# Performance work log

Measured on AMD Instinct MI355X. Metric: run time of the kernel, lower is better.

## Reference

```python
import jax, jax.numpy as jnp
import numpy as np

HEADS = 16
DIM_HEAD = 64
SCALE = DIM_HEAD ** -0.5
MASK_NEG = 1000000.0


def setup_inputs() -> dict:
    key = jax.random.key(0)
    ks = jax.random.split(key, 6)
    B, N, M, D = 2, 2048, 2048, 1024
    inner = HEADS * DIM_HEAD  # 1024
    x = jax.random.normal(ks[0], (B, N, D), dtype=jnp.float32)
    context = jax.random.normal(ks[1], (B, M, D), dtype=jnp.float32)
    mask = jax.random.randint(ks[2], (B, N), 0, 2, dtype=jnp.int32)
    Wq = jax.random.normal(ks[3], (D, inner), dtype=jnp.float32) * (D ** -0.5)
    Wkv = jax.random.normal(ks[4], (D, 2 * inner), dtype=jnp.float32) * (D ** -0.5)
    Wout = jax.random.normal(ks[5], (inner, D), dtype=jnp.float32) * (inner ** -0.5)
    bout = jnp.zeros((D,), dtype=jnp.float32)
    return {"x": x, "context": context, "mask": mask,
            "Wq": Wq, "Wkv": Wkv, "Wout": Wout, "bout": bout}


def _split_heads(t):
    # [b, n, (h d)] -> [b, h, n, d]
    b, n, _ = t.shape
    return t.reshape(b, n, HEADS, DIM_HEAD).transpose(0, 2, 1, 3)


def reference(x, context, mask, Wq, Wkv, Wout, bout):
    kv = context @ Wkv                      # [b, m, 2*inner]
    k, v = jnp.split(kv, 2, axis=-1)
    q = x @ Wq                              # [b, n, inner]
    q, k, v = _split_heads(q), _split_heads(k), _split_heads(v)
    dots = jnp.einsum('bhnd,bhmd->bhnm', q, k) * SCALE
    # mask is [b, n]: additive penalty per query row (faithful to source)
    dots = dots - (1.0 - mask.astype(jnp.float32))[:, None, :, None] * MASK_NEG
    attn = jax.nn.softmax(dots, axis=-1)
    out = jnp.einsum('bhnm,bhmd->bhnd', attn, v)  # [b, h, n, d]
    b, h, n, d = out.shape
    out = out.transpose(0, 2, 1, 3).reshape(b, n, h * d)
    return out @ Wout + bout
```

## Files before the change

### kernel.cpp

```cpp
#include <hip/hip_runtime.h>
#include <hip/hip_bf16.h>
#include <math.h>

#define BATCH   2
#define NQ      2048
#define NKV     2048
#define DMODEL  1024
#define HEADS   16
#define INNER   1024
#define KVCOLS  2048

typedef short bf16x8 __attribute__((ext_vector_type(8)));
typedef float f32x4  __attribute__((ext_vector_type(4)));

__device__ __forceinline__ short f2bf(float x) {
    __hip_bfloat16 h = __float2bfloat16(x);
    return *reinterpret_cast<short*>(&h);
}
__device__ __forceinline__ float bf2f(short h) {
    unsigned int u = ((unsigned int)(unsigned short)h) << 16;
    float f;
    __builtin_memcpy(&f, &u, 4);
    return f;
}
__device__ __forceinline__ void gl_lds16(const void* g, void* l) {
    __builtin_amdgcn_global_load_lds(
        (const __attribute__((address_space(1))) unsigned int*)g,
        (__attribute__((address_space(3))) unsigned int*)l, 16, 0, 0);
}
__device__ __forceinline__ int sw(int row, int chunk) {
    return row * 64 + ((chunk ^ (row & 7)) << 3);
}

__device__ __forceinline__ void split_chunk(const float* __restrict__ in,
                                            short* __restrict__ hi,
                                            short* __restrict__ lo, int id)
{
    const int i = (id * 256 + (int)threadIdx.x) * 4;
    float4 v = *(const float4*)(in + i);
    short4 h, l;
    h.x = f2bf(v.x); l.x = f2bf(v.x - bf2f(h.x));
    h.y = f2bf(v.y); l.y = f2bf(v.y - bf2f(h.y));
    h.z = f2bf(v.z); l.z = f2bf(v.z - bf2f(h.z));
    h.w = f2bf(v.w); l.w = f2bf(v.w - bf2f(h.w));
    *(short4*)(hi + i) = h;
    *(short4*)(lo + i) = l;
}

__device__ __forceinline__ void tile_transpose_split(
    const float* __restrict__ W, short* __restrict__ Wth, short* __restrict__ Wtl,
    int Kd, int Nd, int bx, int by, int split)
{
    __shared__ float t[32][33];
    const int lx = threadIdx.x & 31, ly = threadIdx.x >> 5;
    #pragma unroll
    for (int j = 0; j < 4; ++j)
        t[ly + j * 8][lx] = W[(size_t)(by * 32 + ly + j * 8) * Nd + bx * 32 + lx];
    __syncthreads();
    #pragma unroll
    for (int j = 0; j < 4; ++j) {
        const float v = t[lx][ly + j * 8];
        const short h = f2bf(v);
        const size_t idx = (size_t)(bx * 32 + ly + j * 8) * Kd + by * 32 + lx;
        Wth[idx] = h;
        if (split) Wtl[idx] = f2bf(v - bf2f(h));
    }
}

__global__ __launch_bounds__(256)
void prep_all(const float* __restrict__ x, const float* __restrict__ ctx,
              const float* __restrict__ Wq, const float* __restrict__ Wkv,
              const float* __restrict__ Wout,
              short* __restrict__ xh, short* __restrict__ xl,
              short* __restrict__ ch, short* __restrict__ cl,
              short* __restrict__ WqTh, short* __restrict__ WqTl,
              short* __restrict__ WkvTh, short* __restrict__ WkvTl,
              short* __restrict__ WoutT)
{
    const int id = blockIdx.x;
    if (id < 4096) {
        split_chunk(x, xh, xl, id);
    } else if (id < 8192) {
        split_chunk(ctx, ch, cl, id - 4096);
    } else {
        const int r = id - 8192;
        if (r < 1024)
            tile_transpose_split(Wq, WqTh, WqTl, 1024, 1024, r & 31, r >> 5, 1);
        else if (r < 3072)
            tile_transpose_split(Wkv, WkvTh, WkvTl, 1024, 2048, (r - 1024) & 63, (r - 1024) >> 6, 1);
        else
            tile_transpose_split(Wout, WoutT, nullptr, 1024, 1024, (r - 3072) & 31, (r - 3072) >> 5, 0);
    }
}

__global__ __launch_bounds__(256)
void qkv_gemm(const short* __restrict__ xh, const short* __restrict__ xl,
              const short* __restrict__ ch, const short* __restrict__ cl,
              const short* __restrict__ WqTh, const short* __restrict__ WqTl,
              const short* __restrict__ WkvTh, const short* __restrict__ WkvTl,
              short* __restrict__ qhp, short* __restrict__ qlp,
              short* __restrict__ khp, short* __restrict__ klp,
              short* __restrict__ vp)
{
    __shared__ short Ash[128 * 32];
    __shared__ short Asl[128 * 32];
    __shared__ short Bsh[128 * 32];
    __shared__ short Bsl[128 * 32];

    const int tid = threadIdx.x;
    const int z = blockIdx.z;
    const int m0 = blockIdx.y * 128, n0 = blockIdx.x * 128;
    const int w = tid >> 6, ln = tid & 63;
    const int wm = (w & 1) * 64, wn = (w >> 1) * 64;
    const int lr = ln & 15, lq = ln >> 4;
    const int terms = (z == 2) ? 1 : 3;

    const short* Ah  = (z == 0) ? xh : ch;
    const short* Al  = (z == 0) ? xl : cl;
    const short* Bth = (z == 0) ? WqTh : (z == 1 ? WkvTh : WkvTh + (size_t)1024 * 1024);
    const short* Btl = (z == 0) ? WqTl : WkvTl;

    f32x4 acc[4][4];
    #pragma unroll
    for (int mt = 0; mt < 4; ++mt)
        #pragma unroll
        for (int nt = 0; nt < 4; ++nt)
            #pragma unroll
            for (int r = 0; r < 4; ++r) acc[mt][nt][r] = 0.0f;

    for (int k0 = 0; k0 < 1024; k0 += 32) {
        __syncthreads();
        #pragma unroll
        for (int it = 0; it < 2; ++it) {
            const int f = it * 256 + tid;
            const int row = f >> 2, c = f & 3;
            const int cg = c ^ ((row >> 1) & 3);
            const size_t ao = (size_t)(m0 + row) * 1024 + k0 + cg * 8;
            const size_t bo = (size_t)(n0 + row) * 1024 + k0 + cg * 8;
            gl_lds16(Ah  + ao, Ash + f * 8);
            gl_lds16(Bth + bo, Bsh + f * 8);
            if (terms == 3) {
                gl_lds16(Al  + ao, Asl + f * 8);
                gl_lds16(Btl + bo, Bsl + f * 8);
            }
        }
        __syncthreads();

        bf16x8 ah[4], bh[4];
        #pragma unroll
        for (int t = 0; t < 4; ++t) {
            const int ar = wm + t * 16 + lr;
            const int br = wn + t * 16 + lr;
            ah[t] = *(const bf16x8*)(Ash + ar * 32 + ((lq ^ ((ar >> 1) & 3)) << 3));
            bh[t] = *(const bf16x8*)(Bsh + br * 32 + ((lq ^ ((br >> 1) & 3)) << 3));
        }
        #pragma unroll
        for (int mt = 0; mt < 4; ++mt)
            #pragma unroll
            for (int nt = 0; nt < 4; ++nt)
                acc[mt][nt] = __builtin_amdgcn_mfma_f32_16x16x32_bf16(
                    ah[mt], bh[nt], acc[mt][nt], 0, 0, 0);

        if (terms == 3) {
            bf16x8 al[4], bl[4];
            #pragma unroll
            for (int t = 0; t < 4; ++t) {
                const int ar = wm + t * 16 + lr;
                const int br = wn + t * 16 + lr;
                al[t] = *(const bf16x8*)(Asl + ar * 32 + ((lq ^ ((ar >> 1) & 3)) << 3));
                bl[t] = *(const bf16x8*)(Bsl + br * 32 + ((lq ^ ((br >> 1) & 3)) << 3));
            }
            #pragma unroll
            for (int mt = 0; mt < 4; ++mt)
                #pragma unroll
                for (int nt = 0; nt < 4; ++nt) {
                    acc[mt][nt] = __builtin_amdgcn_mfma_f32_16x16x32_bf16(
                        ah[mt], bl[nt], acc[mt][nt], 0, 0, 0);
                    acc[mt][nt] = __builtin_amdgcn_mfma_f32_16x16x32_bf16(
                        al[mt], bh[nt], acc[mt][nt], 0, 0, 0);
                }
        }
    }

    const float scale = (z == 0) ? 2.0f : 1.0f;
    short* Chi = (z == 0) ? qhp : (z == 1 ? khp : vp);
    short* Clo = (z == 0) ? qlp : klp;
    #pragma unroll
    for (int mt = 0; mt < 4; ++mt)
        #pragma unroll
        for (int nt = 0; nt < 4; ++nt)
            #pragma unroll
            for (int r = 0; r < 4; ++r) {
                const int row = m0 + wm + mt * 16 + lq * 4 + r;
                const int col = n0 + wn + nt * 16 + lr;
                const float v = acc[mt][nt][r] * scale;
                const short hh = f2bf(v);
                Chi[(size_t)row * 1024 + col] = hh;
                if (z != 2)
                    Clo[(size_t)row * 1024 + col] = f2bf(v - bf2f(hh));
            }
}

__global__ __launch_bounds__(256)
void gemm_out(const short* __restrict__ A, const short* __restrict__ Bt,
              float* __restrict__ C, const float* __restrict__ bias)
{
    __shared__ short As[128 * 64];
    __shared__ short Bs[64 * 64];
    const int tid = threadIdx.x;
    const int m0 = blockIdx.y * 128, n0 = blockIdx.x * 64;
    const int w = tid >> 6, ln = tid & 63;
    const int wm = (w & 1) * 64, wn = (w >> 1) * 32;
    const int lr = ln & 15, lq = ln >> 4;

    f32x4 acc[4][2];
    #pragma unroll
    for (int mt = 0; mt < 4; ++mt)
        #pragma unroll
        for (int nt = 0; nt < 2; ++nt)
            #pragma unroll
            for (int r = 0; r < 4; ++r) acc[mt][nt][r] = 0.0f;

    for (int k0 = 0; k0 < 1024; k0 += 64) {
        __syncthreads();
        #pragma unroll
        for (int it = 0; it < 4; ++it) {
            const int f = it * 256 + tid;
            const int row = f >> 3, c8 = f & 7;
            const int cg = c8 ^ (row & 7);
            gl_lds16(A + (size_t)(m0 + row) * 1024 + k0 + cg * 8, As + f * 8);
        }
        #pragma unroll
        for (int it = 0; it < 2; ++it) {
            const int f = it * 256 + tid;
            const int row = f >> 3, c8 = f & 7;
            const int cg = c8 ^ (row & 7);
            gl_lds16(Bt + (size_t)(n0 + row) * 1024 + k0 + cg * 8, Bs + f * 8);
        }
        __syncthreads();
        #pragma unroll
        for (int ks = 0; ks < 2; ++ks) {
            bf16x8 af[4], bfr[2];
            #pragma unroll
            for (int t = 0; t < 4; ++t) {
                const int ar = wm + t * 16 + lr;
                af[t] = *(const bf16x8*)(As + ar * 64 + (((ks * 4 + lq) ^ (ar & 7)) << 3));
            }
            #pragma unroll
            for (int t = 0; t < 2; ++t) {
                const int br = wn + t * 16 + lr;
                bfr[t] = *(const bf16x8*)(Bs + br * 64 + (((ks * 4 + lq) ^ (br & 7)) << 3));
            }
            #pragma unroll
            for (int mt = 0; mt < 4; ++mt)
                #pragma unroll
                for (int nt = 0; nt < 2; ++nt)
                    acc[mt][nt] = __builtin_amdgcn_mfma_f32_16x16x32_bf16(
                        af[mt], bfr[nt], acc[mt][nt], 0, 0, 0);
        }
    }
    #pragma unroll
    for (int mt = 0; mt < 4; ++mt)
        #pragma unroll
        for (int nt = 0; nt < 2; ++nt)
            #pragma unroll
            for (int r = 0; r < 4; ++r) {
                const int row = m0 + wm + mt * 16 + lq * 4 + r;
                const int col = n0 + wn + nt * 16 + lr;
                C[(size_t)row * 1024 + col] = acc[mt][nt][r] + bias[col];
            }
}

__device__ __forceinline__ void vwrite(int* __restrict__ vt32, int dg4, int slot,
                                       int2 a, int2 b)
{
    const short* as = (const short*)&a;
    const short* bs = (const short*)&b;
    #pragma unroll
    for (int j = 0; j < 4; ++j)
        vt32[(dg4 + j) * 32 + (((slot >> 2) ^ ((dg4 + j) & 7)) << 2) + (slot & 3)] =
            (int)((unsigned short)as[j] | ((unsigned int)(unsigned short)bs[j] << 16));
}

__global__ __launch_bounds__(512, 4)
void flash_v9(const short* __restrict__ qh, const short* __restrict__ ql,
              const short* __restrict__ kh, const short* __restrict__ kl,
              const short* __restrict__ vp, const int* __restrict__ mask,
              short* __restrict__ aob)
{
    const int qt = blockIdx.x, h = blockIdx.y, b = blockIdx.z;
    const int tid = threadIdx.x;
    const int w = tid >> 6, ln = tid & 63;
    const int lr = ln & 15, lq = ln >> 4;
    const int kw = w & 1, wq = w >> 1;

    __shared__ short lds[32768];
    short* Kh = lds;
    short* Kl = lds + 8192;
    short* Vt = lds + 16384;
    short* Ps = lds + 24576;

    const size_t qrow0 = (size_t)(b * NQ + qt * 128);

    bf16x8 aqh[2][2], aql[2][2];
    #pragma unroll
    for (int m = 0; m < 2; ++m)
        #pragma unroll
        for (int ks = 0; ks < 2; ++ks) {
            const size_t qoff = (qrow0 + wq * 32 + m * 16 + lr) * INNER + h * 64 + ks * 32 + lq * 8;
            aqh[m][ks] = *(const bf16x8*)(qh + qoff);
            aql[m][ks] = *(const bf16x8*)(ql + qoff);
        }
    float bmag[2][4];
    #pragma unroll
    for (int m = 0; m < 2; ++m)
        #pragma unroll
        for (int r = 0; r < 4; ++r)
            bmag[m][r] = mask[b * NQ + qt * 128 + wq * 32 + m * 16 + lq * 4 + r]
                         ? 0.0f : 12582912.0f;

    bf16x8 vone;
    #pragma unroll
    for (int j = 0; j < 8; ++j) vone[j] = (short)0x3F80;

    const int krow = tid >> 3, kc = tid & 7;
    const int kcg = kc ^ (krow & 7);
    const size_t koff0 = ((size_t)(b * NKV + krow)) * INNER + h * 64 + kcg * 8;

    const int idx = tid & 31, dg4 = (tid >> 5) * 4;
    const int vj  = (idx & 15) + ((idx >> 4) << 5);
    int2 rva, rvb;

    {
        const short* v0 = vp + (size_t)(b * NKV + vj) * INNER + h * 64 + dg4;
        rva = *(const int2*)(v0);
        rvb = *(const int2*)(v0 + 16 * INNER);
        gl_lds16(kh + koff0, Kh + tid * 8);
        gl_lds16(kl + koff0, Kl + tid * 8);
        vwrite((int*)Vt, dg4, idx, rva, rvb);
    }

    f32x4 oacc[2][4];
    #pragma unroll
    for (int m = 0; m < 2; ++m)
        #pragma unroll
        for (int dg = 0; dg < 4; ++dg)
            #pragma unroll
            for (int r = 0; r < 4; ++r) oacc[m][dg][r] = 0.0f;
    f32x4 pacc[2];
    #pragma unroll
    for (int m = 0; m < 2; ++m)
        #pragma unroll
        for (int r = 0; r < 4; ++r) pacc[m][r] = 0.0f;

    const float C16 = 1.44269504f * 0.0625f;
    const int wbase = w * 1024;

    for (int kt = 0; kt < NKV / 64; ++kt) {
        const int cur = kt & 1;
        __syncthreads();

        if (kt < NKV / 64 - 1) {
            const size_t kadd = (size_t)((kt + 1) * 64) * INNER;
            const short* v0 = vp + (size_t)(b * NKV + (kt + 1) * 64 + vj) * INNER + h * 64 + dg4;
            rva = *(const int2*)(v0);
            rvb = *(const int2*)(v0 + 16 * INNER);
            const int nb = (cur ^ 1) * 4096;
            gl_lds16(kh + koff0 + kadd, Kh + nb + tid * 8);
            gl_lds16(kl + koff0 + kadd, Kl + nb + tid * 8);
        }

        const short* KhC = Kh + cur * 4096;
        const short* KlC = Kl + cur * 4096;
        const short* VtC = Vt + cur * 4096;

        f32x4 sacc[2][2];
        #pragma unroll
        for (int m = 0; m < 2; ++m)
            #pragma unroll
            for (int g = 0; g < 2; ++g)
                #pragma unroll
                for (int r = 0; r < 4; ++r) sacc[m][g][r] = 0.0f;
        #pragma unroll
        for (int ks = 0; ks < 2; ++ks) {
            #pragma unroll
            for (int g = 0; g < 2; ++g) {
                const int gg = kw * 2 + g;
                const bf16x8 bkh = *(const bf16x8*)(KhC + sw(gg * 16 + lr, ks * 4 + lq));
                const bf16x8 bkl = *(const bf16x8*)(KlC + sw(gg * 16 + lr, ks * 4 + lq));
                #pragma unroll
                for (int m = 0; m < 2; ++m) {
                    sacc[m][g] = __builtin_amdgcn_mfma_f32_16x16x32_bf16(aqh[m][ks], bkh, sacc[m][g], 0, 0, 0);
                    sacc[m][g] = __builtin_amdgcn_mfma_f32_16x16x32_bf16(aqh[m][ks], bkl, sacc[m][g], 0, 0, 0);
                    sacc[m][g] = __builtin_amdgcn_mfma_f32_16x16x32_bf16(aql[m][ks], bkh, sacc[m][g], 0, 0, 0);
                }
            }
        }

        #pragma unroll
        for (int m = 0; m < 2; ++m)
            #pragma unroll
            for (int r = 0; r < 4; ++r) {
                const int row32 = m * 16 + lq * 4 + r;
                unsigned int pw = 0;
                #pragma unroll
                for (int g = 0; g < 2; ++g) {
                    const float sq = (sacc[m][g][r] + bmag[m][r]) - bmag[m][r];
                    const float xx = sq * C16;
                    float pv;
                    asm("v_exp_f32 %0, %1" : "=v"(pv) : "v"(xx));
                    pw |= ((unsigned int)(unsigned short)f2bf(pv)) << (g * 16);
                }
                const int addr = wbase + row32 * 32 +
                                 (((lr >> 2) ^ ((row32 >> 1) & 3)) << 3) + (lr & 3) * 2;
                *(int*)(Ps + addr) = (int)pw;
            }

        bf16x8 ap[2];
        #pragma unroll
        for (int m = 0; m < 2; ++m) {
            const int row = m * 16 + lr;
            ap[m] = *(const bf16x8*)(Ps + wbase + row * 32 +
                                     ((lq ^ ((row >> 1) & 3)) << 3));
            pacc[m] = __builtin_amdgcn_mfma_f32_16x16x32_bf16(ap[m], vone, pacc[m], 0, 0, 0);
        }
        #pragma unroll
        for (int dg = 0; dg < 4; ++dg) {
            const bf16x8 bv = *(const bf16x8*)(VtC + sw(dg * 16 + lr, kw * 4 + lq));
            oacc[0][dg] = __builtin_amdgcn_mfma_f32_16x16x32_bf16(ap[0], bv, oacc[0][dg], 0, 0, 0);
            oacc[1][dg] = __builtin_amdgcn_mfma_f32_16x16x32_bf16(ap[1], bv, oacc[1][dg], 0, 0, 0);
        }

        if (kt < NKV / 64 - 1) {
            vwrite((int*)(Vt + (cur ^ 1) * 4096), dg4, idx, rva, rvb);
        }
    }

    __syncthreads();
    {
        float* scr = (float*)lds;
        float* slot = scr + ((size_t)(wq * 64 + ln)) * 40;
        if (kw) {
            #pragma unroll
            for (int m = 0; m < 2; ++m) {
                #pragma unroll
                for (int dg = 0; dg < 4; ++dg)
                    *(f32x4*)(slot + m * 16 + dg * 4) = oacc[m][dg];
                *(f32x4*)(slot + 32 + m * 4) = pacc[m];
            }
        }
        __syncthreads();
        if (!kw) {
            #pragma unroll
            for (int m = 0; m < 2; ++m) {
                #pragma unroll
                for (int dg = 0; dg < 4; ++dg)
                    oacc[m][dg] += *(const f32x4*)(slot + m * 16 + dg * 4);
                pacc[m] += *(const f32x4*)(slot + 32 + m * 4);
            }
            #pragma unroll
            for (int m = 0; m < 2; ++m) {
                float pinv[4];
                #pragma unroll
                for (int r = 0; r < 4; ++r) pinv[r] = 1.0f / pacc[m][r];
                #pragma unroll
                for (int dg = 0; dg < 4; ++dg)
                    #pragma unroll
                    for (int r = 0; r < 4; ++r) {
                        const int row = wq * 32 + m * 16 + lq * 4 + r;
                        aob[(qrow0 + row) * INNER + h * 64 + dg * 16 + lr] =
                            f2bf(oacc[m][dg][r] * pinv[r]);
                    }
            }
        }
    }
}

extern "C" void kernel_launch(void* const* d_in, const int* in_sizes, int n_in,
                              void* d_out, int out_size, void* d_ws, size_t ws_size,
                              hipStream_t stream)
{
    const float* x    = (const float*)d_in[0];
    const float* ctx  = (const float*)d_in[1];
    const int*   mask = (const int*)d_in[2];
    const float* Wq   = (const float*)d_in[3];
    const float* Wkv  = (const float*)d_in[4];
    const float* Wout = (const float*)d_in[5];
    const float* bout = (const float*)d_in[6];
    float* out = (float*)d_out;

    short* base  = (short*)d_ws;
    short* xh    = base;
    short* xl    = base + (size_t)4 * 1024 * 1024;
    short* aob   = xh;
    short* WqTh  = base + (size_t) 8 * 1024 * 1024;
    short* WqTl  = base + (size_t) 9 * 1024 * 1024;
    short* qhp   = base + (size_t)10 * 1024 * 1024;
    short* qlp   = base + (size_t)14 * 1024 * 1024;
    short* WkvTh = base + (size_t)18 * 1024 * 1024;
    short* WkvTl = base + (size_t)20 * 1024 * 1024;
    short* khp   = base + (size_t)22 * 1024 * 1024;
    short* klp   = base + (size_t)26 * 1024 * 1024;
    short* WoutT = base + (size_t)30 * 1024 * 1024;
    short* ch    = base + (size_t)31 * 1024 * 1024;
    short* cl    = base + (size_t)35 * 1024 * 1024;
    short* vp    = base + (size_t)39 * 1024 * 1024;

    const dim3 blk(256);
    prep_all<<<12288, blk, 0, stream>>>(x, ctx, Wq, Wkv, Wout,
                                        xh, xl, ch, cl,
                                        WqTh, WqTl, WkvTh, WkvTl, WoutT);
    qkv_gemm<<<dim3(8, 32, 3), blk, 0, stream>>>(
        xh, xl, ch, cl, WqTh, WqTl, WkvTh, WkvTl,
        qhp, qlp, khp, klp, vp);
    flash_v9<<<dim3(NQ / 128, HEADS, BATCH), dim3(512), 0, stream>>>(
        qhp, qlp, khp, klp, vp, mask, aob);
    gemm_out<<<dim3(1024 / 64, 4096 / 128), blk, 0, stream>>>(
        aob, WoutT, out, bout);
}
```

Before: 275.3 us.

## Keep softmax probabilities in registers by transposing S MFMA and permuting V keys

The QK^T MFMAs now swap their operands, so each lane holds score values whose layout matches the A-operand layout of the PV MFMA. The probabilities are converted to bf16 and packed straight into registers, which removes the LDS round trip for P and its shared buffer. To keep this correct, V rows are loaded with a permuted key order, and the mask bias is indexed per lane row. s_setprio hints are also added around the MFMA blocks. Correctness depends on the key permutation matching the register layout exactly. The smaller LDS footprint could also help occupancy.

```diff
diff --git a/kernel.cpp b/kernel.cpp
--- a/kernel.cpp
+++ b/kernel.cpp
@@ -283,10 +283,10 @@
 }
 
 __global__ __launch_bounds__(512, 4)
-void flash_v9(const short* __restrict__ qh, const short* __restrict__ ql,
-              const short* __restrict__ kh, const short* __restrict__ kl,
-              const short* __restrict__ vp, const int* __restrict__ mask,
-              short* __restrict__ aob)
+void flash_v13(const short* __restrict__ qh, const short* __restrict__ ql,
+               const short* __restrict__ kh, const short* __restrict__ kl,
+               const short* __restrict__ vp, const int* __restrict__ mask,
+               short* __restrict__ aob)
 {
     const int qt = blockIdx.x, h = blockIdx.y, b = blockIdx.z;
     const int tid = threadIdx.x;
@@ -294,11 +294,10 @@
     const int lr = ln & 15, lq = ln >> 4;
     const int kw = w & 1, wq = w >> 1;
 
-    __shared__ short lds[32768];
+    __shared__ short lds[24576];
     short* Kh = lds;
     short* Kl = lds + 8192;
     short* Vt = lds + 16384;
-    short* Ps = lds + 24576;
 
     const size_t qrow0 = (size_t)(b * NQ + qt * 128);
 
@@ -311,13 +310,10 @@
             aqh[m][ks] = *(const bf16x8*)(qh + qoff);
             aql[m][ks] = *(const bf16x8*)(ql + qoff);
         }
-    float bmag[2][4];
+    float bmag[2];
     #pragma unroll
     for (int m = 0; m < 2; ++m)
-        #pragma unroll
-        for (int r = 0; r < 4; ++r)
-            bmag[m][r] = mask[b * NQ + qt * 128 + wq * 32 + m * 16 + lq * 4 + r]
-                         ? 0.0f : 12582912.0f;
+        bmag[m] = mask[b * NQ + qt * 128 + wq * 32 + m * 16 + lr] ? 0.0f : 12582912.0f;
 
     bf16x8 vone;
     #pragma unroll
@@ -328,13 +324,15 @@
     const size_t koff0 = ((size_t)(b * NKV + krow)) * INNER + h * 64 + kcg * 8;
 
     const int idx = tid & 31, dg4 = (tid >> 5) * 4;
-    const int vj  = (idx & 15) + ((idx >> 4) << 5);
+    const int tp = idx & 15;
+    const int vkey = ((tp >> 2) << 2) + 2 * (tp & 1) + (((tp >> 1) & 1) << 4)
+                   + ((idx >> 4) << 5);
     int2 rva, rvb;
 
     {
-        const short* v0 = vp + (size_t)(b * NKV + vj) * INNER + h * 64 + dg4;
+        const short* v0 = vp + (size_t)(b * NKV + vkey) * INNER + h * 64 + dg4;
         rva = *(const int2*)(v0);
-        rvb = *(const int2*)(v0 + 16 * INNER);
+        rvb = *(const int2*)(v0 + INNER);
         gl_lds16(kh + koff0, Kh + tid * 8);
         gl_lds16(kl + koff0, Kl + tid * 8);
         vwrite((int*)Vt, dg4, idx, rva, rvb);
@@ -354,7 +352,6 @@
         for (int r = 0; r < 4; ++r) pacc[m][r] = 0.0f;
 
     const float C16 = 1.44269504f * 0.0625f;
-    const int wbase = w * 1024;
 
     for (int kt = 0; kt < NKV / 64; ++kt) {
         const int cur = kt & 1;
@@ -362,9 +359,9 @@
 
         if (kt < NKV / 64 - 1) {
             const size_t kadd = (size_t)((kt + 1) * 64) * INNER;
-            const short* v0 = vp + (size_t)(b * NKV + (kt + 1) * 64 + vj) * INNER + h * 64 + dg4;
+            const short* v0 = vp + (size_t)(b * NKV + (kt + 1) * 64 + vkey) * INNER + h * 64 + dg4;
             rva = *(const int2*)(v0);
-            rvb = *(const int2*)(v0 + 16 * INNER);
+            rvb = *(const int2*)(v0 + INNER);
             const int nb = (cur ^ 1) * 4096;
             gl_lds16(kh + koff0 + kadd, Kh + nb + tid * 8);
             gl_lds16(kl + koff0 + kadd, Kl + nb + tid * 8);
@@ -378,58 +375,55 @@
         #pragma unroll
         for (int m = 0; m < 2; ++m)
             #pragma unroll
-            for (int g = 0; g < 2; ++g)
-                #pragma unroll
-                for (int r = 0; r < 4; ++r) sacc[m][g][r] = 0.0f;
+            for (int g2 = 0; g2 < 2; ++g2)
+                #pragma unroll
+                for (int r = 0; r < 4; ++r) sacc[m][g2][r] = 0.0f;
+        __builtin_amdgcn_s_setprio(1);
         #pragma unroll
         for (int ks = 0; ks < 2; ++ks) {
             #pragma unroll
-            for (int g = 0; g < 2; ++g) {
-                const int gg = kw * 2 + g;
+            for (int g2 = 0; g2 < 2; ++g2) {
+                const int gg = kw * 2 + g2;
                 const bf16x8 bkh = *(const bf16x8*)(KhC + sw(gg * 16 + lr, ks * 4 + lq));
                 const bf16x8 bkl = *(const bf16x8*)(KlC + sw(gg * 16 + lr, ks * 4 + lq));
                 #pragma unroll
                 for (int m = 0; m < 2; ++m) {
-                    sacc[m][g] = __builtin_amdgcn_mfma_f32_16x16x32_bf16(aqh[m][ks], bkh, sacc[m][g], 0, 0, 0);
-                    sacc[m][g] = __builtin_amdgcn_mfma_f32_16x16x32_bf16(aqh[m][ks], bkl, sacc[m][g], 0, 0, 0);
-                    sacc[m][g] = __builtin_amdgcn_mfma_f32_16x16x32_bf16(aql[m][ks], bkh, sacc[m][g], 0, 0, 0);
+                    sacc[m][g2] = __builtin_amdgcn_mfma_f32_16x16x32_bf16(bkh, aqh[m][ks], sacc[m][g2], 0, 0, 0);
+                    sacc[m][g2] = __builtin_amdgcn_mfma_f32_16x16x32_bf16(bkl, aqh[m][ks], sacc[m][g2], 0, 0, 0);
+                    sacc[m][g2] = __builtin_amdgcn_mfma_f32_16x16x32_bf16(bkh, aql[m][ks], sacc[m][g2], 0, 0, 0);
                 }
             }
         }
-
-        #pragma unroll
-        for (int m = 0; m < 2; ++m)
-            #pragma unroll
-            for (int r = 0; r < 4; ++r) {
-                const int row32 = m * 16 + lq * 4 + r;
-                unsigned int pw = 0;
-                #pragma unroll
-                for (int g = 0; g < 2; ++g) {
-                    const float sq = (sacc[m][g][r] + bmag[m][r]) - bmag[m][r];
+        __builtin_amdgcn_s_setprio(0);
+
+        bf16x8 ap[2];
+        #pragma unroll
+        for (int m = 0; m < 2; ++m) {
+            bf16x8 a;
+            #pragma unroll
+            for (int g2 = 0; g2 < 2; ++g2)
+                #pragma unroll
+                for (int r = 0; r < 4; ++r) {
+                    const float sq = (sacc[m][g2][r] + bmag[m]) - bmag[m];
                     const float xx = sq * C16;
                     float pv;
                     asm("v_exp_f32 %0, %1" : "=v"(pv) : "v"(xx));
-                    pw |= ((unsigned int)(unsigned short)f2bf(pv)) << (g * 16);
+                    a[g2 * 4 + r] = f2bf(pv);
                 }
-                const int addr = wbase + row32 * 32 +
-                                 (((lr >> 2) ^ ((row32 >> 1) & 3)) << 3) + (lr & 3) * 2;
-                *(int*)(Ps + addr) = (int)pw;
-            }
-
-        bf16x8 ap[2];
-        #pragma unroll
-        for (int m = 0; m < 2; ++m) {
-            const int row = m * 16 + lr;
-            ap[m] = *(const bf16x8*)(Ps + wbase + row * 32 +
-                                     ((lq ^ ((row >> 1) & 3)) << 3));
+            ap[m] = a;
+        }
+
+        __builtin_amdgcn_s_setprio(1);
+        #pragma unroll
+        for (int m = 0; m < 2; ++m)
             pacc[m] = __builtin_amdgcn_mfma_f32_16x16x32_bf16(ap[m], vone, pacc[m], 0, 0, 0);
-        }
         #pragma unroll
         for (int dg = 0; dg < 4; ++dg) {
             const bf16x8 bv = *(const bf16x8*)(VtC + sw(dg * 16 + lr, kw * 4 + lq));
             oacc[0][dg] = __builtin_amdgcn_mfma_f32_16x16x32_bf16(ap[0], bv, oacc[0][dg], 0, 0, 0);
             oacc[1][dg] = __builtin_amdgcn_mfma_f32_16x16x32_bf16(ap[1], bv, oacc[1][dg], 0, 0, 0);
         }
+        __builtin_amdgcn_s_setprio(0);
 
         if (kt < NKV / 64 - 1) {
             vwrite((int*)(Vt + (cur ^ 1) * 4096), dg4, idx, rva, rvb);
@@ -439,7 +433,7 @@
     __syncthreads();
     {
         float* scr = (float*)lds;
-        float* slot = scr + ((size_t)(wq * 64 + ln)) * 40;
+        float* slot = scr + (size_t)(wq * 64 + ln) * 40;
         if (kw) {
             #pragma unroll
             for (int m = 0; m < 2; ++m) {
@@ -513,7 +507,7 @@
     qkv_gemm<<<dim3(8, 32, 3), blk, 0, stream>>>(
         xh, xl, ch, cl, WqTh, WqTl, WkvTh, WkvTl,
         qhp, qlp, khp, klp, vp);
-    flash_v9<<<dim3(NQ / 128, HEADS, BATCH), dim3(512), 0, stream>>>(
+    flash_v13<<<dim3(NQ / 128, HEADS, BATCH), dim3(512), 0, stream>>>(
         qhp, qlp, khp, klp, vp, mask, aob);
     gemm_out<<<dim3(1024 / 64, 4096 / 128), blk, 0, stream>>>(
         aob, WoutT, out, bout);
```

After: 254.4 us. 1.08x faster.
